# Optimization experiments

Measured on AMD Instinct MI355X. Metric: run time of the kernel, lower is better.

Reference implementation:

```python
import jax, jax.numpy as jnp
import numpy as np

NVOC = 32000
DIM = 512
HID = 512
NLAYERS = 2
SEQ = 128
BATCH = 32


def setup_inputs() -> dict:
    key = jax.random.key(0)
    ks = jax.random.split(key, 8)
    tokens = jax.random.randint(ks[0], (SEQ, BATCH), 0, NVOC, dtype=jnp.int32)
    emb = jax.random.uniform(ks[1], (NVOC, DIM), minval=-0.1, maxval=0.1, dtype=jnp.float32)
    # xavier-uniform-ish init for gate matrices
    def xav(k, shape):
        fan_in, fan_out = shape[1], shape[0]
        lim = jnp.sqrt(6.0 / (fan_in + fan_out))
        return jax.random.uniform(k, shape, minval=-lim, maxval=lim, dtype=jnp.float32)
    W0 = xav(ks[2], (4 * HID, DIM))     # layer 0 input weights
    W1 = xav(ks[3], (4 * HID, HID))     # layer 1 input weights
    U0 = xav(ks[4], (4 * HID, HID))
    U1 = xav(ks[5], (4 * HID, HID))
    b = jnp.zeros((4 * HID,), jnp.float32)
    dec_w = jax.random.uniform(ks[6], (NVOC, HID), minval=-0.1, maxval=0.1, dtype=jnp.float32)
    dec_b = jnp.zeros((NVOC,), jnp.float32)
    return {"tokens": tokens, "emb": emb, "W0": W0, "W1": W1,
            "U0": U0, "U1": U1, "b": b, "dec_w": dec_w, "dec_b": dec_b}


def _lstm_forward(tokens, emb, W0, W1, U0, U1, b, dec_w, dec_b):
    # dropout in eval mode (identity)
    x = emb[tokens]  # [S, B, DIM]
    Ws = [W0, W1]
    Us = [U0, U1]
    h0 = jnp.zeros((NLAYERS, BATCH, HID), x.dtype)
    c0 = jnp.zeros((NLAYERS, BATCH, HID), x.dtype)

    def step(carry, x_t):
        h_tot, c_tot = carry
        new_h, new_c = [], []
        inp = x_t
        for l in range(NLAYERS):
            gates = inp @ Ws[l].T + h_tot[l] @ Us[l].T + b  # [B, 4H]
            i_g, f_g, g_g, o_g = jnp.split(gates, 4, axis=1)
            i_g = jax.nn.sigmoid(i_g)
            f_g = jax.nn.sigmoid(f_g)
            o_g = jax.nn.sigmoid(o_g)
            g_g = jnp.tanh(g_g)
            c_new = f_g * c_tot[l] + i_g * g_g
            h_new = o_g * jnp.tanh(c_new)
            new_h.append(h_new)
            new_c.append(c_new)
            inp = h_new
        return (jnp.stack(new_h), jnp.stack(new_c)), new_h[-1]

    (_, _), outs = jax.lax.scan(step, (h0, c0), x)  # outs: [S, B, HID]
    decoded = outs @ dec_w.T + dec_b  # [S, B, NVOC]
    return decoded


def reference(tokens, emb, W0, W1, U0, U1, b, dec_w, dec_b):
    return _lstm_forward(tokens, emb, W0, W1, U0, U1, b, dec_w, dec_b)
```

## Files before the change

kernel.cpp:

```cpp
#include <hip/hip_runtime.h>
#include <hip/hip_bf16.h>


#define NVOC 32000
#define DIM  512
#define HID  512
#define SEQ  128
#define BAT  32
#define NB   64
#define NDEC 192
#define NTILE (32 * 250)
#define SLOT (BAT * HID)

typedef short s8v __attribute__((ext_vector_type(8)));
typedef short s4v __attribute__((ext_vector_type(4)));
typedef float f4v __attribute__((ext_vector_type(4)));
typedef unsigned long long u64;

__device__ __forceinline__ short f2bf(float f) {
    unsigned u = __builtin_bit_cast(unsigned, f);
    unsigned r = (u + 0x7fffu + ((u >> 16) & 1u)) >> 16;
    return (short)r;
}
__device__ __forceinline__ float bf2f(short s) {
    unsigned u = ((unsigned)(unsigned short)s) << 16;
    return __builtin_bit_cast(float, u);
}
__device__ __forceinline__ float sigm(float x) { return 1.f / (1.f + __expf(-x)); }
__device__ __forceinline__ float ftanh(float x) {
    float e = __expf(2.f * x);
    return 1.f - 2.f / (e + 1.f);
}

__device__ __forceinline__ f4v mf16(s8v a, s8v b, f4v c) {
    return __builtin_amdgcn_mfma_f32_16x16x32_bf16(a, b, c, 0, 0, 0);
}

__device__ __forceinline__ u64 cohload8(const short* p) {
    return __hip_atomic_load((const u64*)p, __ATOMIC_RELAXED,
                             __HIP_MEMORY_SCOPE_AGENT);
}
__device__ __forceinline__ void cohstore4(short* p, unsigned v) {
    __hip_atomic_store((unsigned*)p, v, __ATOMIC_RELAXED,
                       __HIP_MEMORY_SCOPE_AGENT);
}

__device__ __forceinline__ bool hasSent(u64 v) {
    u64 n = ~v;
    return ((n - 0x0001000100010001ull) & ~n & 0x8000800080008000ull) != 0ull;
}

__device__ __forceinline__ void poll32s(const unsigned* f, int l, unsigned tgt) {
    const unsigned* p = f + (l & 31);
    while (true) {
        unsigned v = __hip_atomic_load(p, __ATOMIC_RELAXED,
                                       __HIP_MEMORY_SCOPE_AGENT);
        if (__all((int)(v >= tgt))) break;
        __builtin_amdgcn_s_sleep(16);
    }
}

__global__ __launch_bounds__(256) void prep_all(
    const float* __restrict__ dw, short* __restrict__ dbf,
    const float* __restrict__ W0, short* __restrict__ w0h,
    short* __restrict__ w0l,
    const int* __restrict__ toks, const float* __restrict__ emb,
    short* __restrict__ xemb,
    short* __restrict__ hbuf, unsigned* __restrict__ bar)
{
    const int b = blockIdx.x, tid = threadIdx.x;
    if (b < 16000) {
        int id = b * 256 + tid;
        int e = id * 4;
        float4 v = *(const float4*)(dw + e);
        s4v o; o[0] = f2bf(v.x); o[1] = f2bf(v.y); o[2] = f2bf(v.z); o[3] = f2bf(v.w);
        *(s4v*)(dbf + e) = o;
    } else if (b < 20096) {
        int id = (b - 16000) * 256 + tid;
        float v = W0[id];
        short h = f2bf(v);
        w0h[id] = h;
        w0l[id] = f2bf(v - bf2f(h));
    } else if (b < 22144) {
        int id = (b - 20096) * 256 + tid;
        int e  = id * 4;
        int tb = e >> 9;
        int k4 = e & 511;
        int tok = toks[tb];
        float4 v = *(const float4*)(emb + (size_t)tok * DIM + k4);
        s4v o; o[0] = f2bf(v.x); o[1] = f2bf(v.y); o[2] = f2bf(v.z); o[3] = f2bf(v.w);
        *(s4v*)(xemb + e) = o;
    } else {
        int id = (b - 22144) * 256 + tid;
        const int ringU64 = 129 * SLOT / 4;
        if (id < 2 * ringU64) {
            int r = id % ringU64;
            u64 v = (r < SLOT / 4) ? 0ull : 0xFFFFFFFFFFFFFFFFull;
            ((u64*)hbuf)[id] = v;
        }
        if (id < 64) bar[id] = 0;
    }
}

__global__ __launch_bounds__(256) void gx_gemm(
    const short* __restrict__ A,
    const short* __restrict__ Bh,
    const short* __restrict__ Bl,
    float* __restrict__ out)
{
    const int nb = blockIdx.x & 15, mb = blockIdx.x >> 4;
    const int m0 = mb * 128, n0 = nb * 128;
    __shared__ short Alds[128][40];
    __shared__ short Bhl[128][40];
    __shared__ short Bll[128][40];
    const int tid = threadIdx.x, l = tid & 63, w = tid >> 6;
    const int wr = w >> 1, wc = w & 1;
    const int lr = l & 15, kg = l >> 4;

    f4v acc[4][4];
    #pragma unroll
    for (int mi = 0; mi < 4; ++mi)
        #pragma unroll
        for (int ni = 0; ni < 4; ++ni) {
            acc[mi][ni][0] = 0.f; acc[mi][ni][1] = 0.f;
            acc[mi][ni][2] = 0.f; acc[mi][ni][3] = 0.f;
        }

    for (int kt = 0; kt < 16; ++kt) {
        #pragma unroll
        for (int i = 0; i < 2; ++i) {
            int c = tid + i * 256;
            int row = c >> 2, q = (c & 3) << 3;
            *(s8v*)&Alds[row][q] = *(const s8v*)(A  + (size_t)(m0 + row) * 512 + kt * 32 + q);
            *(s8v*)&Bhl[row][q]  = *(const s8v*)(Bh + (size_t)(n0 + row) * 512 + kt * 32 + q);
            *(s8v*)&Bll[row][q]  = *(const s8v*)(Bl + (size_t)(n0 + row) * 512 + kt * 32 + q);
        }
        __syncthreads();
        s8v af[4], bhf[4], blf[4];
        #pragma unroll
        for (int i = 0; i < 4; ++i) {
            af[i]  = *(const s8v*)&Alds[wr * 64 + i * 16 + lr][kg * 8];
            bhf[i] = *(const s8v*)&Bhl[wc * 64 + i * 16 + lr][kg * 8];
            blf[i] = *(const s8v*)&Bll[wc * 64 + i * 16 + lr][kg * 8];
        }
        #pragma unroll
        for (int mi = 0; mi < 4; ++mi)
            #pragma unroll
            for (int ni = 0; ni < 4; ++ni) {
                acc[mi][ni] = mf16(af[mi], bhf[ni], acc[mi][ni]);
                acc[mi][ni] = mf16(af[mi], blf[ni], acc[mi][ni]);
            }
        __syncthreads();
    }

    #pragma unroll
    for (int mi = 0; mi < 4; ++mi)
        #pragma unroll
        for (int ni = 0; ni < 4; ++ni) {
            int n = n0 + wc * 64 + ni * 16 + lr;
            #pragma unroll
            for (int r = 0; r < 4; ++r) {
                int m = m0 + wr * 64 + mi * 16 + kg * 4 + r;
                out[(size_t)m * 2048 + n] = acc[mi][ni][r];
            }
        }
}

__global__ __launch_bounds__(512, 1) void rnn_k(
    const float* __restrict__ W1f, const float* __restrict__ U0f,
    const float* __restrict__ U1f,
    const float* __restrict__ bias,
    const float* __restrict__ Gx,
    short* __restrict__ hbuf,
    short* __restrict__ adec,
    const short* __restrict__ dbf,
    const float* __restrict__ db,
    float* __restrict__ out,
    unsigned* __restrict__ bar)
{
    const int tid = threadIdx.x;
    const int bx  = blockIdx.x;
    const int w2  = tid >> 6;
    const int l   = tid & 63;
    const int lr  = l & 15;
    const int kg  = l >> 4;

    __shared__ short Alds[32][520];
    __shared__ float gbuf[2][4][16][33];
    __shared__ float pbuf[2][4][16][33];
    __shared__ s8v AdT[4][132];
    __shared__ s8v BdT[4][132];

    if (bx >= NB) {
        const int d  = bx - NB;
        const int wm = w2 >> 2;
        const int wn = w2 & 3;
        const int drow = tid >> 2, dq = tid & 3;
        int lastmb = -1;
        for (int tile = d; tile < NTILE; tile += NDEC) {
            const int mb = tile / 250, nbt = tile - mb * 250;
            const int m0 = mb * 128, n0 = nbt * 128;
            if (mb != lastmb) {
                if (w2 == 0) poll32s(bar + 32, l, (unsigned)(4 * mb + 5));
                __syncthreads();
                lastmb = mb;
            }
            f4v acc[4][2];
            #pragma unroll
            for (int mi = 0; mi < 4; ++mi)
                #pragma unroll
                for (int ni = 0; ni < 2; ++ni) {
                    acc[mi][ni][0] = 0.f; acc[mi][ni][1] = 0.f;
                    acc[mi][ni][2] = 0.f; acc[mi][ni][3] = 0.f;
                }
            for (int kt = 0; kt < 16; ++kt) {
                AdT[dq][drow] = *(const s8v*)(adec + (size_t)(m0 + drow) * 512 + kt * 32 + dq * 8);
                BdT[dq][drow] = *(const s8v*)(dbf  + (size_t)(n0 + drow) * 512 + kt * 32 + dq * 8);
                __syncthreads();
                s8v af[4], bfr[2];
                #pragma unroll
                for (int i = 0; i < 4; ++i)
                    af[i] = AdT[kg][wm * 64 + i * 16 + lr];
                #pragma unroll
                for (int j = 0; j < 2; ++j)
                    bfr[j] = BdT[kg][wn * 32 + j * 16 + lr];
                #pragma unroll
                for (int mi = 0; mi < 4; ++mi)
                    #pragma unroll
                    for (int ni = 0; ni < 2; ++ni)
                        acc[mi][ni] = mf16(af[mi], bfr[ni], acc[mi][ni]);
                __syncthreads();
            }
            #pragma unroll
            for (int mi = 0; mi < 4; ++mi)
                #pragma unroll
                for (int ni = 0; ni < 2; ++ni) {
                    int n = n0 + wn * 32 + ni * 16 + lr;
                    float bb = db[n];
                    #pragma unroll
                    for (int r = 0; r < 4; ++r) {
                        int m = m0 + wm * 64 + mi * 16 + kg * 4 + r;
                        out[(size_t)m * NVOC + n] = acc[mi][ni][r] + bb;
                    }
                }
        }
        return;
    }

    const int bl    = bx;
    const int layer = bl >> 5;
    const int j0    = (bl & 31) * 16;

    const bool epi = (tid < 256);
    const int eb  = (tid >> 3) & 31;
    const int ej  = (tid & 7) * 2;
    const int jg0 = j0 + ej;
    float bi0 = 0, bi1 = 0, bff0 = 0, bff1 = 0, bg0 = 0, bg1 = 0, bo0 = 0, bo1 = 0;
    if (epi) {
        bi0 = bias[jg0];         bi1 = bias[jg0 + 1];
        bff0 = bias[512 + jg0];  bff1 = bias[512 + jg0 + 1];
        bg0 = bias[1024 + jg0];  bg1 = bias[1024 + jg0 + 1];
        bo0 = bias[1536 + jg0];  bo1 = bias[1536 + jg0 + 1];
    }
    float c0 = 0.f, c1 = 0.f;

    short* ring0 = hbuf;
    short* ring1 = hbuf + 129 * SLOT;

    auto stageS = [&](const short* s) {
        u64 va[8];
        #pragma unroll
        for (int i = 0; i < 8; ++i) {
            int c = tid + i * 512;
            va[i] = cohload8(s + (c >> 7) * HID + (c & 127) * 4);
        }
        #pragma unroll
        for (int i = 0; i < 8; ++i) {
            int c = tid + i * 512;
            while (hasSent(va[i]))
                va[i] = cohload8(s + (c >> 7) * HID + (c & 127) * 4);
            *(u64*)&Alds[c >> 7][(c & 127) * 4] = va[i];
        }
    };
    const int g  = w2 & 3;
    const int kh = w2 >> 2;
    auto mfma8 = [&](const s8v* WH, const s8v* WL, float (&dst)[2][4][16][33]) {
        f4v a0h = {0.f, 0.f, 0.f, 0.f};
        f4v a0l = a0h, a1h = a0h, a1l = a0h;
        #pragma unroll
        for (int ks = 0; ks < 8; ++ks) {
            const int k = kh * 256 + ks * 32 + kg * 8;
            s8v a0 = *(const s8v*)&Alds[lr][k];
            s8v a1 = *(const s8v*)&Alds[16 + lr][k];
            a0h = mf16(a0, WH[ks], a0h);
            a0l = mf16(a0, WL[ks], a0l);
            a1h = mf16(a1, WH[ks], a1h);
            a1l = mf16(a1, WL[ks], a1l);
        }
        #pragma unroll
        for (int r = 0; r < 4; ++r) {
            dst[kh][g][lr][kg * 4 + r]      = a0h[r] + a0l[r];
            dst[kh][g][lr][16 + kg * 4 + r] = a1h[r] + a1l[r];
        }
    };
    const int gr = g * 512 + j0 + lr;
    auto loadw = [&](const float* M, s8v* WH, s8v* WL) {
        #pragma unroll
        for (int ks = 0; ks < 8; ++ks) {
            const float* src = M + (size_t)gr * 512 + kh * 256 + ks * 32 + kg * 8;
            float4 va = *(const float4*)src;
            float4 vb = *(const float4*)(src + 4);
            float vv[8] = {va.x, va.y, va.z, va.w, vb.x, vb.y, vb.z, vb.w};
            s8v hi, lo;
            #pragma unroll
            for (int e = 0; e < 8; ++e) {
                short h = f2bf(vv[e]);
                hi[e] = h; lo[e] = f2bf(vv[e] - bf2f(h));
            }
            WH[ks] = hi; WL[ks] = lo;
        }
    };

    if (layer == 0) {
        s8v wh[8], wl[8];
        loadw(U0f, wh, wl);
        for (int it = 0; it < SEQ; ++it) {
            float2 gxv0 = {0, 0}, gxv1 = {0, 0}, gxv2 = {0, 0}, gxv3 = {0, 0};
            if (epi) {
                const float* gp = Gx + ((size_t)it * BAT + eb) * 2048 + jg0;
                gxv0 = *(const float2*)(gp);
                gxv1 = *(const float2*)(gp + 512);
                gxv2 = *(const float2*)(gp + 1024);
                gxv3 = *(const float2*)(gp + 1536);
            }
            stageS(ring0 + (size_t)it * SLOT);
            __syncthreads();
            mfma8(wh, wl, gbuf);
            __syncthreads();
            if (epi) {
                float si0 = gbuf[0][0][ej][eb]     + gbuf[1][0][ej][eb]     + gxv0.x;
                float si1 = gbuf[0][0][ej + 1][eb] + gbuf[1][0][ej + 1][eb] + gxv0.y;
                float sf0 = gbuf[0][1][ej][eb]     + gbuf[1][1][ej][eb]     + gxv1.x;
                float sf1 = gbuf[0][1][ej + 1][eb] + gbuf[1][1][ej + 1][eb] + gxv1.y;
                float sg0 = gbuf[0][2][ej][eb]     + gbuf[1][2][ej][eb]     + gxv2.x;
                float sg1 = gbuf[0][2][ej + 1][eb] + gbuf[1][2][ej + 1][eb] + gxv2.y;
                float so0 = gbuf[0][3][ej][eb]     + gbuf[1][3][ej][eb]     + gxv3.x;
                float so1 = gbuf[0][3][ej + 1][eb] + gbuf[1][3][ej + 1][eb] + gxv3.y;
                float gi0 = sigm(si0 + bi0), gi1 = sigm(si1 + bi1);
                float gf0 = sigm(sf0 + bff0), gf1 = sigm(sf1 + bff1);
                float gg0 = ftanh(sg0 + bg0), gg1 = ftanh(sg1 + bg1);
                float go0 = sigm(so0 + bo0), go1 = sigm(so1 + bo1);
                c0 = gf0 * c0 + gi0 * gg0;
                c1 = gf1 * c1 + gi1 * gg1;
                unsigned hw = (unsigned)(unsigned short)f2bf(go0 * ftanh(c0)) |
                              ((unsigned)(unsigned short)f2bf(go1 * ftanh(c1)) << 16);
                cohstore4(ring0 + (size_t)(it + 1) * SLOT + eb * HID + jg0, hw);
            }
        }
    } else {
        s8v whU[8], wlU[8], whW[8], wlW[8];
        loadw(U1f, whU, wlU);
        loadw(W1f, whW, wlW);
        stageS(ring0 + 1 * SLOT);
        __syncthreads();
        mfma8(whW, wlW, pbuf);
        __syncthreads();
        for (int it = 1; it <= SEQ; ++it) {
            stageS(ring1 + (size_t)(it - 1) * SLOT);
            __syncthreads();
            mfma8(whU, wlU, gbuf);
            __syncthreads();
            unsigned hw = 0;
            if (epi) {
                float si0 = gbuf[0][0][ej][eb]     + gbuf[1][0][ej][eb]
                          + pbuf[0][0][ej][eb]     + pbuf[1][0][ej][eb];
                float si1 = gbuf[0][0][ej + 1][eb] + gbuf[1][0][ej + 1][eb]
                          + pbuf[0][0][ej + 1][eb] + pbuf[1][0][ej + 1][eb];
                float sf0 = gbuf[0][1][ej][eb]     + gbuf[1][1][ej][eb]
                          + pbuf[0][1][ej][eb]     + pbuf[1][1][ej][eb];
                float sf1 = gbuf[0][1][ej + 1][eb] + gbuf[1][1][ej + 1][eb]
                          + pbuf[0][1][ej + 1][eb] + pbuf[1][1][ej + 1][eb];
                float sg0 = gbuf[0][2][ej][eb]     + gbuf[1][2][ej][eb]
                          + pbuf[0][2][ej][eb]     + pbuf[1][2][ej][eb];
                float sg1 = gbuf[0][2][ej + 1][eb] + gbuf[1][2][ej + 1][eb]
                          + pbuf[0][2][ej + 1][eb] + pbuf[1][2][ej + 1][eb];
                float so0 = gbuf[0][3][ej][eb]     + gbuf[1][3][ej][eb]
                          + pbuf[0][3][ej][eb]     + pbuf[1][3][ej][eb];
                float so1 = gbuf[0][3][ej + 1][eb] + gbuf[1][3][ej + 1][eb]
                          + pbuf[0][3][ej + 1][eb] + pbuf[1][3][ej + 1][eb];
                float gi0 = sigm(si0 + bi0), gi1 = sigm(si1 + bi1);
                float gf0 = sigm(sf0 + bff0), gf1 = sigm(sf1 + bff1);
                float gg0 = ftanh(sg0 + bg0), gg1 = ftanh(sg1 + bg1);
                float go0 = sigm(so0 + bo0), go1 = sigm(so1 + bo1);
                c0 = gf0 * c0 + gi0 * gg0;
                c1 = gf1 * c1 + gi1 * gg1;
                hw = (unsigned)(unsigned short)f2bf(go0 * ftanh(c0)) |
                     ((unsigned)(unsigned short)f2bf(go1 * ftanh(c1)) << 16);
                cohstore4(ring1 + (size_t)it * SLOT + eb * HID + jg0, hw);
                cohstore4(adec + ((size_t)(it - 1) * BAT + eb) * HID + jg0, hw);
            }
            if ((it & 3) == 0 || it == SEQ) {
                asm volatile("s_waitcnt vmcnt(0)" ::: "memory");
                __syncthreads();
                if (tid == 0)
                    __hip_atomic_store(bar + 32 + (bl & 31), (unsigned)(it + 1),
                                       __ATOMIC_RELAXED, __HIP_MEMORY_SCOPE_AGENT);
            }
            if (it < SEQ) {
                stageS(ring0 + (size_t)(it + 1) * SLOT);
                __syncthreads();
                mfma8(whW, wlW, pbuf);
                __syncthreads();
            }
        }
    }
}

extern "C" void kernel_launch(void* const* d_in, const int* in_sizes, int n_in,
                              void* d_out, int out_size, void* d_ws, size_t ws_size,
                              hipStream_t stream)
{
    const int*   toks = (const int*)d_in[0];
    const float* emb  = (const float*)d_in[1];
    const float* W0   = (const float*)d_in[2];
    const float* W1   = (const float*)d_in[3];
    const float* U0   = (const float*)d_in[4];
    const float* U1   = (const float*)d_in[5];
    const float* bias = (const float*)d_in[6];
    const float* dw   = (const float*)d_in[7];
    const float* db   = (const float*)d_in[8];
    float* out = (float*)d_out;

    char* ws = (char*)d_ws;
    size_t off = 0;
    auto alloc = [&](size_t bytes) -> void* {
        void* p = ws + off;
        off += (bytes + 255) & ~(size_t)255;
        return p;
    };
    short*    dbf  = (short*)alloc((size_t)NVOC * DIM * 2);
    short*    xemb = (short*)alloc((size_t)SEQ * BAT * DIM * 2);
    short*    w0h  = (short*)alloc(2048ull * 512 * 2);
    short*    w0l  = (short*)alloc(2048ull * 512 * 2);
    float*    Gx   = (float*)alloc((size_t)SEQ * BAT * 2048 * 4);
    short*    hbuf = (short*)alloc(2ull * 129 * SLOT * 2);
    short*    adec = (short*)alloc((size_t)SEQ * BAT * HID * 2);
    unsigned* bar  = (unsigned*)alloc(256);

    prep_all<<<26272, 256, 0, stream>>>(dw, dbf, W0, w0h, w0l,
                                        toks, emb, xemb, hbuf, bar);

    gx_gemm<<<32 * 16, 256, 0, stream>>>(xemb, w0h, w0l, Gx);

    rnn_k<<<NB + NDEC, 512, 0, stream>>>(W1, U0, U1, bias, Gx, hbuf, adec,
                                         dbf, db, out, bar);
}
```

Before: 695.5 us.

## Double block size so layer-1 recurrent and input GEMMs run concurrently

Launches the persistent RNN kernel with 1024 threads per block. In layer-1 blocks, warps 0-7 compute the U1·h recurrent product while warps 8-15 compute W1·x from layer 0's output at the same time, each holding only one weight set in registers, instead of running the two products back to back. The decoder blocks split each 128x128 tile over 16 warps with one N fragment each. This shortens the serial per-timestep chain, but it doubles threads per block, changes the launch bounds, and leaves half the warps idle in layer-0 blocks, which may increase register pressure or reduce occupancy.

```diff
diff --git a/kernel.cpp b/kernel.cpp
--- a/kernel.cpp
+++ b/kernel.cpp
@@ -166,7 +166,7 @@
         }
 }
 
-__global__ __launch_bounds__(512, 1) void rnn_k(
+__global__ __launch_bounds__(1024, 4) void rnn_k(
     const float* __restrict__ W1f, const float* __restrict__ U0f,
     const float* __restrict__ U1f,
     const float* __restrict__ bias,
@@ -185,7 +185,7 @@
     const int lr  = l & 15;
     const int kg  = l >> 4;
 
-    __shared__ short Alds[32][520];
+    __shared__ short Alds[32][1032];
     __shared__ float gbuf[2][4][16][33];
     __shared__ float pbuf[2][4][16][33];
     __shared__ s8v AdT[4][132];
@@ -193,8 +193,8 @@
 
     if (bx >= NB) {
         const int d  = bx - NB;
-        const int wm = w2 >> 2;
-        const int wn = w2 & 3;
+        const int wm = w2 >> 3;
+        const int wn = w2 & 7;
         const int drow = tid >> 2, dq = tid & 3;
         int lastmb = -1;
         for (int tile = d; tile < NTILE; tile += NDEC) {
@@ -205,43 +205,36 @@
                 __syncthreads();
                 lastmb = mb;
             }
-            f4v acc[4][2];
+            f4v acc[4];
+            #pragma unroll
+            for (int mi = 0; mi < 4; ++mi) {
+                acc[mi][0] = 0.f; acc[mi][1] = 0.f;
+                acc[mi][2] = 0.f; acc[mi][3] = 0.f;
+            }
+            for (int kt = 0; kt < 16; ++kt) {
+                if (tid < 512) {
+                    AdT[dq][drow] = *(const s8v*)(adec + (size_t)(m0 + drow) * 512 + kt * 32 + dq * 8);
+                    BdT[dq][drow] = *(const s8v*)(dbf  + (size_t)(n0 + drow) * 512 + kt * 32 + dq * 8);
+                }
+                __syncthreads();
+                s8v af[4];
+                #pragma unroll
+                for (int i = 0; i < 4; ++i)
+                    af[i] = AdT[kg][wm * 64 + i * 16 + lr];
+                s8v bf1 = BdT[kg][wn * 16 + lr];
+                #pragma unroll
+                for (int mi = 0; mi < 4; ++mi)
+                    acc[mi] = mf16(af[mi], bf1, acc[mi]);
+                __syncthreads();
+            }
+            int n = n0 + wn * 16 + lr;
+            float bb = db[n];
             #pragma unroll
             for (int mi = 0; mi < 4; ++mi)
                 #pragma unroll
-                for (int ni = 0; ni < 2; ++ni) {
-                    acc[mi][ni][0] = 0.f; acc[mi][ni][1] = 0.f;
-                    acc[mi][ni][2] = 0.f; acc[mi][ni][3] = 0.f;
-                }
-            for (int kt = 0; kt < 16; ++kt) {
-                AdT[dq][drow] = *(const s8v*)(adec + (size_t)(m0 + drow) * 512 + kt * 32 + dq * 8);
-                BdT[dq][drow] = *(const s8v*)(dbf  + (size_t)(n0 + drow) * 512 + kt * 32 + dq * 8);
-                __syncthreads();
-                s8v af[4], bfr[2];
-                #pragma unroll
-                for (int i = 0; i < 4; ++i)
-                    af[i] = AdT[kg][wm * 64 + i * 16 + lr];
-                #pragma unroll
-                for (int j = 0; j < 2; ++j)
-                    bfr[j] = BdT[kg][wn * 32 + j * 16 + lr];
-                #pragma unroll
-                for (int mi = 0; mi < 4; ++mi)
-                    #pragma unroll
-                    for (int ni = 0; ni < 2; ++ni)
-                        acc[mi][ni] = mf16(af[mi], bfr[ni], acc[mi][ni]);
-                __syncthreads();
-            }
-            #pragma unroll
-            for (int mi = 0; mi < 4; ++mi)
-                #pragma unroll
-                for (int ni = 0; ni < 2; ++ni) {
-                    int n = n0 + wn * 32 + ni * 16 + lr;
-                    float bb = db[n];
-                    #pragma unroll
-                    for (int r = 0; r < 4; ++r) {
-                        int m = m0 + wm * 64 + mi * 16 + kg * 4 + r;
-                        out[(size_t)m * NVOC + n] = acc[mi][ni][r] + bb;
-                    }
+                for (int r = 0; r < 4; ++r) {
+                    int m = m0 + wm * 64 + mi * 16 + kg * 4 + r;
+                    out[(size_t)m * NVOC + n] = acc[mi][r] + bb;
                 }
         }
         return;
@@ -250,6 +243,9 @@
     const int bl    = bx;
     const int layer = bl >> 5;
     const int j0    = (bl & 31) * 16;
+    const int w3    = w2 & 7;
+    const int g     = w3 & 3;
+    const int kh    = w3 >> 2;
 
     const bool epi = (tid < 256);
     const int eb  = (tid >> 3) & 31;
@@ -267,29 +263,43 @@
     short* ring0 = hbuf;
     short* ring1 = hbuf + 129 * SLOT;
 
-    auto stageS = [&](const short* s) {
+    auto stage512 = [&](const short* s, int t, int cb) {
         u64 va[8];
         #pragma unroll
         for (int i = 0; i < 8; ++i) {
-            int c = tid + i * 512;
+            int c = t + i * 512;
             va[i] = cohload8(s + (c >> 7) * HID + (c & 127) * 4);
         }
         #pragma unroll
         for (int i = 0; i < 8; ++i) {
-            int c = tid + i * 512;
+            int c = t + i * 512;
+            while (hasSent(va[i]))
+                va[i] = cohload8(s + (c >> 7) * HID + (c & 127) * 4);
+            *(u64*)&Alds[c >> 7][cb + (c & 127) * 4] = va[i];
+        }
+    };
+    auto stage1024 = [&](const short* s) {
+        u64 va[4];
+        #pragma unroll
+        for (int i = 0; i < 4; ++i) {
+            int c = tid + i * 1024;
+            va[i] = cohload8(s + (c >> 7) * HID + (c & 127) * 4);
+        }
+        #pragma unroll
+        for (int i = 0; i < 4; ++i) {
+            int c = tid + i * 1024;
             while (hasSent(va[i]))
                 va[i] = cohload8(s + (c >> 7) * HID + (c & 127) * 4);
             *(u64*)&Alds[c >> 7][(c & 127) * 4] = va[i];
         }
     };
-    const int g  = w2 & 3;
-    const int kh = w2 >> 2;
-    auto mfma8 = [&](const s8v* WH, const s8v* WL, float (&dst)[2][4][16][33]) {
+    auto mfma8 = [&](const s8v* WH, const s8v* WL, int cb,
+                     float (&dst)[2][4][16][33]) {
         f4v a0h = {0.f, 0.f, 0.f, 0.f};
         f4v a0l = a0h, a1h = a0h, a1l = a0h;
         #pragma unroll
         for (int ks = 0; ks < 8; ++ks) {
-            const int k = kh * 256 + ks * 32 + kg * 8;
+            const int k = cb + ks * 32 + kg * 8;
             s8v a0 = *(const s8v*)&Alds[lr][k];
             s8v a1 = *(const s8v*)&Alds[16 + lr][k];
             a0h = mf16(a0, WH[ks], a0h);
@@ -323,7 +333,7 @@
 
     if (layer == 0) {
         s8v wh[8], wl[8];
-        loadw(U0f, wh, wl);
+        if (w2 < 8) loadw(U0f, wh, wl);
         for (int it = 0; it < SEQ; ++it) {
             float2 gxv0 = {0, 0}, gxv1 = {0, 0}, gxv2 = {0, 0}, gxv3 = {0, 0};
             if (epi) {
@@ -333,9 +343,9 @@
                 gxv2 = *(const float2*)(gp + 1024);
                 gxv3 = *(const float2*)(gp + 1536);
             }
-            stageS(ring0 + (size_t)it * SLOT);
+            stage1024(ring0 + (size_t)it * SLOT);
             __syncthreads();
-            mfma8(wh, wl, gbuf);
+            if (w2 < 8) mfma8(wh, wl, kh * 256, gbuf);
             __syncthreads();
             if (epi) {
                 float si0 = gbuf[0][0][ej][eb]     + gbuf[1][0][ej][eb]     + gxv0.x;
@@ -358,19 +368,15 @@
             }
         }
     } else {
-        s8v whU[8], wlU[8], whW[8], wlW[8];
-        loadw(U1f, whU, wlU);
-        loadw(W1f, whW, wlW);
-        stageS(ring0 + 1 * SLOT);
-        __syncthreads();
-        mfma8(whW, wlW, pbuf);
-        __syncthreads();
+        s8v wh[8], wl[8];
+        loadw((w2 < 8) ? U1f : W1f, wh, wl);
         for (int it = 1; it <= SEQ; ++it) {
-            stageS(ring1 + (size_t)(it - 1) * SLOT);
+            if (w2 < 8) stage512(ring1 + (size_t)(it - 1) * SLOT, tid, 0);
+            else        stage512(ring0 + (size_t)it * SLOT, tid - 512, 520);
             __syncthreads();
-            mfma8(whU, wlU, gbuf);
+            if (w2 < 8) mfma8(wh, wl, kh * 256, gbuf);
+            else        mfma8(wh, wl, 520 + kh * 256, pbuf);
             __syncthreads();
-            unsigned hw = 0;
             if (epi) {
                 float si0 = gbuf[0][0][ej][eb]     + gbuf[1][0][ej][eb]
                           + pbuf[0][0][ej][eb]     + pbuf[1][0][ej][eb];
@@ -394,8 +400,8 @@
                 float go0 = sigm(so0 + bo0), go1 = sigm(so1 + bo1);
                 c0 = gf0 * c0 + gi0 * gg0;
                 c1 = gf1 * c1 + gi1 * gg1;
-                hw = (unsigned)(unsigned short)f2bf(go0 * ftanh(c0)) |
-                     ((unsigned)(unsigned short)f2bf(go1 * ftanh(c1)) << 16);
+                unsigned hw = (unsigned)(unsigned short)f2bf(go0 * ftanh(c0)) |
+                              ((unsigned)(unsigned short)f2bf(go1 * ftanh(c1)) << 16);
                 cohstore4(ring1 + (size_t)it * SLOT + eb * HID + jg0, hw);
                 cohstore4(adec + ((size_t)(it - 1) * BAT + eb) * HID + jg0, hw);
             }
@@ -405,12 +411,6 @@
                 if (tid == 0)
                     __hip_atomic_store(bar + 32 + (bl & 31), (unsigned)(it + 1),
                                        __ATOMIC_RELAXED, __HIP_MEMORY_SCOPE_AGENT);
-            }
-            if (it < SEQ) {
-                stageS(ring0 + (size_t)(it + 1) * SLOT);
-                __syncthreads();
-                mfma8(whW, wlW, pbuf);
-                __syncthreads();
             }
         }
     }
@@ -452,6 +452,6 @@
 
     gx_gemm<<<32 * 16, 256, 0, stream>>>(xemb, w0h, w0l, Gx);
 
-    rnn_k<<<NB + NDEC, 512, 0, stream>>>(W1, U0, U1, bias, Gx, hbuf, adec,
-                                         dbf, db, out, bar);
-}
+    rnn_k<<<NB + NDEC, 1024, 0, stream>>>(W1, U0, U1, bias, Gx, hbuf, adec,
+                                          dbf, db, out, bar);
+}
```

Result: slower. 1.097 ms (+57.7%).
